# Kernel optimization log

Measured on AMD Instinct MI355X. Metric: run time of the kernel, lower is better.

## Reference

```python
import jax, jax.numpy as jnp
import numpy as np

# Config mirroring My_MLP(mlp_layers=2, isize=512, k=30, non_linearity='relu',
#                        mlp_act='relu', offset_list=[2048]*4)
SIZES = [2048, 2048, 2048, 2048]   # per-client subgraph sizes (offset_list)
N = sum(SIZES)                      # 8192 total nodes
D = 512                             # isize
K = 30 + 1                          # module uses self.k + 1


def setup_inputs() -> dict:
    key = jax.random.key(0)
    k1, k2, k3 = jax.random.split(key, 3)
    features = jax.random.normal(k1, (N, D), dtype=jnp.float32)
    # Diag layer weights: a learned diagonal (vector) per layer, init near 1.
    w0 = 1.0 + 0.1 * jax.random.normal(k2, (D,), dtype=jnp.float32)
    w1 = 1.0 + 0.1 * jax.random.normal(k3, (D,), dtype=jnp.float32)
    return {"features": features, "w0": w0, "w1": w1}


def reference(features, w0, w1):
    # internal_forward: Diag -> relu -> Diag (no act after last layer)
    h = jax.nn.relu(features * w0) * w1                 # [N, D]
    # F.normalize(dim=1, p=2)
    emb = h * jax.lax.rsqrt(jnp.sum(h * h, axis=1, keepdims=True) + 1e-24)
    sim = jnp.matmul(emb, emb.T)                        # [N, N]

    # cross_subgraph_topk: per row, keep top-(k+1) similarities among columns
    # belonging to a DIFFERENT client subgraph; zero everything else.
    seg = jnp.asarray(np.repeat(np.arange(len(SIZES)), SIZES))   # [N] int
    same = seg[:, None] == seg[None, :]                           # [N, N] bool
    masked = jnp.where(same, -jnp.inf, sim)
    vals, inds = jax.lax.top_k(masked, K)                         # [N, K]
    rows = jnp.arange(N)[:, None]
    out = jnp.zeros_like(sim).at[rows, inds].set(vals)

    # apply_non_linearity('relu', i)
    return jax.nn.relu(out)
```

## Files before the change

kernel.cpp:

```cpp
#include <hip/hip_runtime.h>
#include <hip/hip_bf16.h>
#include <hip/hip_fp16.h>
#include <math.h>

typedef unsigned short u16;
typedef unsigned int u32;
typedef unsigned long long u64;
typedef __attribute__((ext_vector_type(8))) short bf16x8;
typedef __attribute__((ext_vector_type(4))) float f32x4;

#define N_NODES 8192
#define DIM 512
#define KSEL 31
#define BANDCAP 128
#define SEG_SIZE 2048
#define NVALID 6144
#define BAND_ULP 8

__device__ __forceinline__ u32 f16key(u32 h) {
  return (h & 0x8000u) ? (0xFFFFu & ~h) : (h | 0x8000u);
}
__device__ __forceinline__ u32 packkeys(u32 w) {
  return f16key(w & 0xFFFFu) | (f16key(w >> 16) << 16);
}
__device__ __forceinline__ float keyval(u32 k) {
  const u16 raw = (k & 0x8000u) ? (u16)(k ^ 0x8000u) : (u16)(~k & 0xFFFFu);
  __half_raw hr; hr.x = raw;
  return __half2float(__half(hr));
}

#define GLD_LDS16(g, l)                                        \
  __builtin_amdgcn_global_load_lds(                            \
      (const __attribute__((address_space(1))) void*)(g),      \
      (__attribute__((address_space(3))) void*)(l), 16, 0, 0)

__global__ __launch_bounds__(256) void prep_kernel(
    const float* __restrict__ feat, const float* __restrict__ w0,
    const float* __restrict__ w1, u16* __restrict__ embh,
    float* __restrict__ embf, u32* __restrict__ kmax32) {
#pragma clang fp contract(off)
  const int row = blockIdx.x;
  const int t = threadIdx.x;
  __shared__ float hs[DIM];
  __shared__ float partial[32];
  __shared__ float rinv_sh;

  const float2 x = *reinterpret_cast<const float2*>(feat + (size_t)row * DIM + t * 2);
  const float2 a = *reinterpret_cast<const float2*>(w0 + t * 2);
  const float2 b = *reinterpret_cast<const float2*>(w1 + t * 2);
  const float h0 = fmaxf(x.x * a.x, 0.0f) * b.x;
  const float h1 = fmaxf(x.y * a.y, 0.0f) * b.y;
  hs[t * 2] = h0;
  hs[t * 2 + 1] = h1;
  if (t == 0) kmax32[row] = 0u;
  __syncthreads();

  if (t < 32) {
    const int base = (t >> 3) * 128 + (t & 7);
    float v = hs[base];
    float acc = v * v;
    for (int i = 1; i < 16; ++i) {
      v = hs[base + 8 * i];
      const float vv = v * v;
      acc = acc + vv;
    }
    partial[t] = acc;
  }
  __syncthreads();
  if (t == 0) {
    float B[4];
    for (int blk = 0; blk < 4; ++blk) {
      const float* p = &partial[blk * 8];
      B[blk] = ((p[0] + p[1]) + (p[2] + p[3])) + ((p[4] + p[5]) + (p[6] + p[7]));
    }
    const float s = (B[0] + B[1]) + (B[2] + B[3]);
    const float sp = s + 1e-24f;
    const float qf = (float)sqrt((double)sp);
    rinv_sh = (float)(1.0 / (double)qf);
  }
  __syncthreads();
  const float rinv = rinv_sh;
  const float e0 = h0 * rinv;
  const float e1 = h1 * rinv;
  *reinterpret_cast<float2*>(embf + (size_t)row * DIM + t * 2) = make_float2(e0, e1);
  __hip_bfloat162 bb;
  bb.x = __float2bfloat16(e0);
  bb.y = __float2bfloat16(e1);
  *reinterpret_cast<__hip_bfloat162*>(embh + (size_t)row * DIM + t * 2) = bb;
}

__global__ __launch_bounds__(256) void gemm_kernel(const u16* __restrict__ embh,
                                                   __half* __restrict__ simh,
                                                   u32* __restrict__ kmax32) {
  __shared__ u16 As[128][64];
  __shared__ u16 Bs[128][64];
  const int tid = threadIdx.x;
  const int lane = tid & 63;
  const int wave = tid >> 6;
  const int wm = wave >> 1;
  const int wn = wave & 1;
  const int rowTile = blockIdx.y;
  const int segTileBase = (rowTile >> 4) << 4;
  const int cT = blockIdx.x;
  const int colTile = cT < segTileBase ? cT : cT + 16;
  const int row0 = rowTile * 128;
  const int col0 = colTile * 128;

  f32x4 acc[4][4] = {};

  for (int k0 = 0; k0 < DIM; k0 += 64) {
#pragma unroll
    for (int i = 0; i < 4; ++i) {
      const int flat = i * 256 + tid;
      const int r = flat >> 3;
      const int c = (flat & 7) * 8;
      GLD_LDS16(embh + (size_t)(row0 + r) * DIM + k0 + c, &As[r][c]);
      GLD_LDS16(embh + (size_t)(col0 + r) * DIM + k0 + c, &Bs[r][c]);
    }
    __syncthreads();
#pragma unroll
    for (int kk = 0; kk < 2; ++kk) {
      bf16x8 afr[4], bfr[4];
      const int koff = kk * 32 + (lane >> 4) * 8;
      const int rsel = lane & 15;
#pragma unroll
      for (int m = 0; m < 4; ++m)
        afr[m] = *reinterpret_cast<const bf16x8*>(&As[wm * 64 + m * 16 + rsel][koff]);
#pragma unroll
      for (int n = 0; n < 4; ++n)
        bfr[n] = *reinterpret_cast<const bf16x8*>(&Bs[wn * 64 + n * 16 + rsel][koff]);
#pragma unroll
      for (int m = 0; m < 4; ++m)
#pragma unroll
        for (int n = 0; n < 4; ++n)
          acc[m][n] = __builtin_amdgcn_mfma_f32_16x16x32_bf16(afr[m], bfr[n],
                                                              acc[m][n], 0, 0, 0);
    }
    __syncthreads();
  }
#pragma unroll
  for (int m = 0; m < 4; ++m)
#pragma unroll
    for (int n = 0; n < 4; ++n)
#pragma unroll
      for (int j = 0; j < 4; ++j) {
        const int r = row0 + wm * 64 + m * 16 + (lane >> 4) * 4 + j;
        const int pcol = cT * 128 + wn * 64 + n * 16 + (lane & 15);
        simh[(size_t)r * NVALID + pcol] = __float2half(acc[m][n][j]);
      }
#pragma unroll
  for (int m = 0; m < 4; ++m) {
#pragma unroll
    for (int j = 0; j < 4; ++j) {
      float vmax = fmaxf(fmaxf(acc[m][0][j], acc[m][1][j]),
                         fmaxf(acc[m][2][j], acc[m][3][j]));
#pragma unroll
      for (int off = 1; off < 16; off <<= 1)
        vmax = fmaxf(vmax, __shfl_xor(vmax, off, 64));
      if ((lane & 15) == 0) {
        const int r = row0 + wm * 64 + m * 16 + (lane >> 4) * 4 + j;
        const u32 b = __float_as_uint(vmax);
        const u32 kk = (b & 0x80000000u) ? ~b : (b | 0x80000000u);
        atomicMax(&kmax32[r], kk);
      }
    }
  }
}

__global__ __launch_bounds__(256) void select_kernel(
    const __half* __restrict__ simh, const float* __restrict__ embf,
    const u32* __restrict__ kmax32, int2* __restrict__ compact) {
  const int row = blockIdx.x;
  const int t = threadIdx.x;
  const int lane = t & 63;
  const int wave = t >> 6;

  __shared__ u32 hist[257];
  __shared__ int bcol[BANDCAP];
  __shared__ float bex[BANDCAP];
  __shared__ int outidx_s[KSEL];
  __shared__ float outval_s[KSEL];
  __shared__ int cnts[2];
  __shared__ u32 sh_lo, sh_hi, sh_need;
  __shared__ int sh_state;

  const int segBase = (row >> 11) << 11;

  u32 pk[12];
  {
    const uint4* src = reinterpret_cast<const uint4*>(simh + (size_t)row * NVALID);
    const uint4 a = src[t], b = src[256 + t], c = src[512 + t];
    pk[0] = packkeys(a.x); pk[1] = packkeys(a.y);
    pk[2] = packkeys(a.z); pk[3] = packkeys(a.w);
    pk[4] = packkeys(b.x); pk[5] = packkeys(b.y);
    pk[6] = packkeys(b.z); pk[7] = packkeys(b.w);
    pk[8] = packkeys(c.x); pk[9] = packkeys(c.y);
    pk[10] = packkeys(c.z); pk[11] = packkeys(c.w);
  }
#define KEY(v) ((pk[(v) >> 1] >> (((v) & 1) * 16)) & 0xFFFFu)
#define COL(v) ((((((v) >> 3) * 256) + t) << 3) + ((v) & 7))

  if (t < KSEL) { outidx_s[t] = segBase; outval_s[t] = 0.0f; }
  if (t == 0) { cnts[0] = 0; cnts[1] = 0; }

  u32 kmax16;
  {
    const u32 kk = kmax32[row];
    const u32 fb = (kk & 0x80000000u) ? (kk ^ 0x80000000u) : ~kk;
    const __half h = __float2half(__uint_as_float(fb));
    kmax16 = f16key((u32)__half_as_ushort(h));
  }

  u32 base = (kmax16 > 511u) ? kmax16 - 511u : 0u;
  u32 winTop = kmax16;
  u32 shift = 2;
  u32 need = KSEL;
  int tier = 0;
  for (int guard = 0; guard < 6; ++guard) {
    hist[t] = 0;
    if (t == 0) hist[256] = 0;
    __syncthreads();
#pragma unroll
    for (int v = 0; v < 24; ++v) {
      const u32 k = KEY(v);
      if (k >= base && k <= winTop) atomicAdd(&hist[(k - base) >> shift], 1u);
    }
    __syncthreads();
    if (wave == 0) {
      const int x = lane * 4;
      const u32 b0 = hist[x], b1 = hist[x + 1];
      const u32 b2 = hist[x + 2], b3 = hist[x + 3];
      const u32 tot = b0 + b1 + b2 + b3;
      u32 inc = tot;
#pragma unroll
      for (int off = 1; off < 64; off <<= 1) {
        const u32 vv = (u32)__shfl_down((int)inc, off, 64);
        if (lane + off < 64) inc += vv;
      }
      const u32 exc = inc - tot;
      const u32 g3 = exc, g2 = g3 + b3, g1 = g2 + b2, g0 = g1 + b1;
      int sel = -1;
      u32 gsel = 0;
      if (g3 < need && g3 + b3 >= need) { sel = x + 3; gsel = g3; }
      else if (g2 < need && g2 + b2 >= need) { sel = x + 2; gsel = g2; }
      else if (g1 < need && g1 + b1 >= need) { sel = x + 1; gsel = g1; }
      else if (g0 < need && g0 + b0 >= need) { sel = x;     gsel = g0; }
      const u64 bal = __ballot(sel >= 0);
      if (lane == 0 && bal == 0) sh_state = 0;
      if (bal != 0) {
        const int srcl = (int)(__ffsll((unsigned long long)bal) - 1);
        sel  = __shfl(sel, srcl, 64);
        gsel = (u32)__shfl((int)gsel, srcl, 64);
        if (lane == 0) {
          const u32 blo = base + ((u32)sel << shift);
          const u32 bhi = min(blo + (1u << shift) - 1u, winTop);
          sh_lo = blo; sh_hi = bhi; sh_need = need - gsel;
          sh_state = (shift > 2) ? 1 : 2;
        }
      }
    }
    __syncthreads();
    const int st = sh_state;
    if (st == 2) break;
    if (st == 1) {
      base = sh_lo; winTop = sh_hi; shift = 0; need = sh_need;
    } else {
      ++tier;
      if (tier == 1) { base = (kmax16 > 8191u) ? kmax16 - 8191u : 0u; shift = 5; }
      else { base = 0u; shift = 8; }
      winTop = kmax16; need = KSEL;
    }
    __syncthreads();
  }
  const u32 binlo = sh_lo, binhi = sh_hi;
  const u32 hiK = binhi + BAND_ULP;
  const u32 loK = (binlo >= BAND_ULP) ? binlo - BAND_ULP : 0u;

#pragma unroll
  for (int v = 0; v < 24; ++v) {
    const u32 k = KEY(v);
    if (k > hiK) {
      const int slot = atomicAdd(&cnts[1], 1);
      const int i = COL(v);
      if (slot < KSEL) {
        outidx_s[slot] = (i < segBase) ? i : i + SEG_SIZE;
        outval_s[slot] = fmaxf(keyval(k), 0.0f);
      }
    } else if (k >= loK) {
      const int slot = atomicAdd(&cnts[0], 1);
      const int i = COL(v);
      if (slot < BANDCAP) bcol[slot] = (i < segBase) ? i : i + SEG_SIZE;
    }
  }
  __syncthreads();
  const int nH = min(cnts[1], KSEL);
  const int slots = KSEL - nH;
  const int nB = min(cnts[0], BANDCAP);

  if (t < nB) {
#pragma clang fp contract(off)
    const float4* g4 =
        reinterpret_cast<const float4*>(embf + (size_t)bcol[t] * DIM);
    const float4* e4 = reinterpret_cast<const float4*>(embf + (size_t)row * DIM);
    float acc = 0.0f;
    for (int k4 = 0; k4 < DIM / 4; ++k4) {
      const float4 a = e4[k4];
      const float4 b = g4[k4];
      acc = acc + a.x * b.x;
      acc = acc + a.y * b.y;
      acc = acc + a.z * b.z;
      acc = acc + a.w * b.w;
    }
    bex[t] = acc;
  }
  __syncthreads();

  if (t < nB) {
    const float ev = bex[t];
    const int ec = bcol[t];
    int r = 0;
    for (int j = 0; j < nB; ++j) {
      const float oj = bex[j];
      const int cj = bcol[j];
      if (oj > ev || (oj == ev && cj < ec)) r++;
    }
    if (r < slots) {
      const int slot = atomicAdd(&cnts[1], 1);
      if (slot < KSEL) { outidx_s[slot] = ec; outval_s[slot] = fmaxf(ev, 0.0f); }
    }
  }
  __syncthreads();
  if (t < KSEL)
    compact[(size_t)row * KSEL + t] =
        make_int2(outidx_s[t], __float_as_int(outval_s[t]));
#undef KEY
#undef COL
}

__global__ __launch_bounds__(256) void write_kernel(
    const int2* __restrict__ compact, float* __restrict__ out) {
  const int row = blockIdx.x;
  const int t = threadIdx.x;
  __shared__ int sidx[KSEL];
  __shared__ float sval[KSEL];
  if (t < KSEL) {
    const int2 e = compact[(size_t)row * KSEL + t];
    sidx[t] = e.x;
    sval[t] = __int_as_float(e.y);
  }
  float* orow = out + (size_t)row * N_NODES;
  const float4 zero4 = make_float4(0.f, 0.f, 0.f, 0.f);
  __syncthreads();
#pragma unroll
  for (int i = 0; i < 8; ++i)
    reinterpret_cast<float4*>(orow)[i * 256 + t] = zero4;
  __syncthreads();
  if (t < KSEL) orow[sidx[t]] = sval[t];
}

extern "C" void kernel_launch(void* const* d_in, const int* in_sizes, int n_in,
                              void* d_out, int out_size, void* d_ws, size_t ws_size,
                              hipStream_t stream) {
  const float* feat = (const float*)d_in[0];
  const float* w0 = (const float*)d_in[1];
  const float* w1 = (const float*)d_in[2];
  float* out = (float*)d_out;

  u16* embh = (u16*)d_ws;
  float* embf = (float*)((char*)d_ws + (size_t)N_NODES * DIM * 2);
  u32* kmax32 = (u32*)((char*)d_ws + (size_t)24 * 1024 * 1024);
  int2* compact = (int2*)d_ws;
  __half* simh = (__half*)d_out;

  prep_kernel<<<N_NODES, 256, 0, stream>>>(feat, w0, w1, embh, embf, kmax32);
  dim3 grid(48, 64);
  gemm_kernel<<<grid, 256, 0, stream>>>(embh, simh, kmax32);
  select_kernel<<<N_NODES, 256, 0, stream>>>(simh, embf, kmax32, compact);
  write_kernel<<<N_NODES, 256, 0, stream>>>(compact, out);
}
```

Baseline: 246.3 us.

## Refine top-k histogram windows, skip fp32 rescoring when band fits, split zero/scatter

The first histogram tier now uses exact 1-ULP bins over a 256-key window, and the fallback tier is narrowed. This makes it more likely that the threshold bin is resolved without a second refinement pass. When the candidate band exactly fills the remaining slots, the fp32 dot-product rescoring and ranking are skipped and fp16 keys are used directly. That risks small value differences against the fp32 reference. The per-row write kernel is replaced by a grid-stride zero kernel plus a flat scatter kernel, which adds a launch in exchange for simpler memory streaming.

Result: slower. 258.4 us (+4.9%).

```diff
diff --git a/kernel.cpp b/kernel.cpp
--- a/kernel.cpp
+++ b/kernel.cpp
@@ -177,6 +177,7 @@
 
   __shared__ u32 hist[257];
   __shared__ int bcol[BANDCAP];
+  __shared__ u32 bkey[BANDCAP];
   __shared__ float bex[BANDCAP];
   __shared__ int outidx_s[KSEL];
   __shared__ float outval_s[KSEL];
@@ -211,9 +212,9 @@
     kmax16 = f16key((u32)__half_as_ushort(h));
   }
 
-  u32 base = (kmax16 > 511u) ? kmax16 - 511u : 0u;
+  u32 base = (kmax16 > 255u) ? kmax16 - 255u : 0u;
   u32 winTop = kmax16;
-  u32 shift = 2;
+  u32 shift = 0;
   u32 need = KSEL;
   int tier = 0;
   for (int guard = 0; guard < 6; ++guard) {
@@ -255,7 +256,7 @@
           const u32 blo = base + ((u32)sel << shift);
           const u32 bhi = min(blo + (1u << shift) - 1u, winTop);
           sh_lo = blo; sh_hi = bhi; sh_need = need - gsel;
-          sh_state = (shift > 2) ? 1 : 2;
+          sh_state = (shift > 0) ? 1 : 2;
         }
       }
     }
@@ -266,7 +267,7 @@
       base = sh_lo; winTop = sh_hi; shift = 0; need = sh_need;
     } else {
       ++tier;
-      if (tier == 1) { base = (kmax16 > 8191u) ? kmax16 - 8191u : 0u; shift = 5; }
+      if (tier == 1) { base = (kmax16 > 2047u) ? kmax16 - 2047u : 0u; shift = 3; }
       else { base = 0u; shift = 8; }
       winTop = kmax16; need = KSEL;
     }
@@ -289,7 +290,10 @@
     } else if (k >= loK) {
       const int slot = atomicAdd(&cnts[0], 1);
       const int i = COL(v);
-      if (slot < BANDCAP) bcol[slot] = (i < segBase) ? i : i + SEG_SIZE;
+      if (slot < BANDCAP) {
+        bcol[slot] = (i < segBase) ? i : i + SEG_SIZE;
+        bkey[slot] = k;
+      }
     }
   }
   __syncthreads();
@@ -297,36 +301,45 @@
   const int slots = KSEL - nH;
   const int nB = min(cnts[0], BANDCAP);
 
-  if (t < nB) {
+  if (nB == slots) {
+    if (t < nB) {
+      const int slot = atomicAdd(&cnts[1], 1);
+      if (slot < KSEL) {
+        outidx_s[slot] = bcol[t];
+        outval_s[slot] = fmaxf(keyval(bkey[t]), 0.0f);
+      }
+    }
+  } else {
+    if (t < nB) {
 #pragma clang fp contract(off)
-    const float4* g4 =
-        reinterpret_cast<const float4*>(embf + (size_t)bcol[t] * DIM);
-    const float4* e4 = reinterpret_cast<const float4*>(embf + (size_t)row * DIM);
-    float acc = 0.0f;
-    for (int k4 = 0; k4 < DIM / 4; ++k4) {
-      const float4 a = e4[k4];
-      const float4 b = g4[k4];
-      acc = acc + a.x * b.x;
-      acc = acc + a.y * b.y;
-      acc = acc + a.z * b.z;
-      acc = acc + a.w * b.w;
-    }
-    bex[t] = acc;
-  }
-  __syncthreads();
-
-  if (t < nB) {
-    const float ev = bex[t];
-    const int ec = bcol[t];
-    int r = 0;
-    for (int j = 0; j < nB; ++j) {
-      const float oj = bex[j];
-      const int cj = bcol[j];
-      if (oj > ev || (oj == ev && cj < ec)) r++;
-    }
-    if (r < slots) {
-      const int slot = atomicAdd(&cnts[1], 1);
-      if (slot < KSEL) { outidx_s[slot] = ec; outval_s[slot] = fmaxf(ev, 0.0f); }
+      const float4* g4 =
+          reinterpret_cast<const float4*>(embf + (size_t)bcol[t] * DIM);
+      const float4* e4 = reinterpret_cast<const float4*>(embf + (size_t)row * DIM);
+      float acc = 0.0f;
+      for (int k4 = 0; k4 < DIM / 4; ++k4) {
+        const float4 a = e4[k4];
+        const float4 b = g4[k4];
+        acc = acc + a.x * b.x;
+        acc = acc + a.y * b.y;
+        acc = acc + a.z * b.z;
+        acc = acc + a.w * b.w;
+      }
+      bex[t] = acc;
+    }
+    __syncthreads();
+    if (t < nB) {
+      const float ev = bex[t];
+      const int ec = bcol[t];
+      int r = 0;
+      for (int j = 0; j < nB; ++j) {
+        const float oj = bex[j];
+        const int cj = bcol[j];
+        if (oj > ev || (oj == ev && cj < ec)) r++;
+      }
+      if (r < slots) {
+        const int slot = atomicAdd(&cnts[1], 1);
+        if (slot < KSEL) { outidx_s[slot] = ec; outval_s[slot] = fmaxf(ev, 0.0f); }
+      }
     }
   }
   __syncthreads();
@@ -337,25 +350,21 @@
 #undef COL
 }
 
-__global__ __launch_bounds__(256) void write_kernel(
+__global__ __launch_bounds__(256) void zero_kernel(float4* __restrict__ out4) {
+  const size_t total = (size_t)N_NODES * N_NODES / 4;
+  const float4 z = make_float4(0.f, 0.f, 0.f, 0.f);
+  for (size_t i = (size_t)blockIdx.x * 256 + threadIdx.x; i < total;
+       i += (size_t)gridDim.x * 256)
+    out4[i] = z;
+}
+
+__global__ __launch_bounds__(256) void scatter_kernel(
     const int2* __restrict__ compact, float* __restrict__ out) {
-  const int row = blockIdx.x;
-  const int t = threadIdx.x;
-  __shared__ int sidx[KSEL];
-  __shared__ float sval[KSEL];
-  if (t < KSEL) {
-    const int2 e = compact[(size_t)row * KSEL + t];
-    sidx[t] = e.x;
-    sval[t] = __int_as_float(e.y);
-  }
-  float* orow = out + (size_t)row * N_NODES;
-  const float4 zero4 = make_float4(0.f, 0.f, 0.f, 0.f);
-  __syncthreads();
-#pragma unroll
-  for (int i = 0; i < 8; ++i)
-    reinterpret_cast<float4*>(orow)[i * 256 + t] = zero4;
-  __syncthreads();
-  if (t < KSEL) orow[sidx[t]] = sval[t];
+  const int gid = blockIdx.x * 256 + threadIdx.x;
+  if (gid >= N_NODES * KSEL) return;
+  const int row = gid / KSEL;
+  const int2 e = compact[gid];
+  out[(size_t)row * N_NODES + e.x] = __int_as_float(e.y);
 }
 
 extern "C" void kernel_launch(void* const* d_in, const int* in_sizes, int n_in,
@@ -374,7 +383,8 @@
 
   prep_kernel<<<N_NODES, 256, 0, stream>>>(feat, w0, w1, embh, embf, kmax32);
   dim3 grid(48, 64);
-  gemm_kernel<<<grid, 256, 0, stream>>>(embh, simh, kmax32);
+  gemm_kernel<<<grid, 64 * 4, 0, stream>>>(embh, simh, kmax32);
   select_kernel<<<N_NODES, 256, 0, stream>>>(simh, embf, kmax32, compact);
-  write_kernel<<<N_NODES, 256, 0, stream>>>(compact, out);
-}
+  zero_kernel<<<2048, 256, 0, stream>>>((float4*)out);
+  scatter_kernel<<<(N_NODES * KSEL + 255) / 256, 256, 0, stream>>>(compact, out);
+}
```
